# Kernel tuning notes

Measured on AMD Instinct MI355X. Metric: run time of the kernel, lower is better.

The kernel has to match this reference:

```python
import jax, jax.numpy as jnp
import numpy as np

T, B, D, H = 512, 64, 1024, 8
DH = D // H
LN_EPS = 1e-5


def setup_inputs() -> dict:
    ks = jax.random.split(jax.random.key(0), 12)
    s = 1.0 / np.sqrt(D)
    return {
        "x_real": jax.random.normal(ks[0], (T, B, D), jnp.float32),
        "x_imag": jax.random.normal(ks[1], (T, B, D), jnp.float32),
        "value_state": jnp.zeros((B, H, DH), jnp.float32),
        "t": jnp.arange(T, dtype=jnp.int64) if jax.config.jax_enable_x64 else jnp.arange(T, dtype=jnp.int32),
        # ComplexLinear input_proj (bias=True): weight layout [out, in] like torch
        "Wr_in": jax.random.normal(ks[2], (D, D), jnp.float32) * s,
        "Wi_in": jax.random.normal(ks[3], (D, D), jnp.float32) * s,
        "br_in": jax.random.normal(ks[4], (D,), jnp.float32) * 0.01,
        "bi_in": jax.random.normal(ks[5], (D,), jnp.float32) * 0.01,
        # LayerNorm affine
        "ln_gamma": jnp.ones((D,), jnp.float32),
        "ln_beta": jnp.zeros((D,), jnp.float32),
        # QKV linear (bias=False), torch layout [3D, D]
        "W_qkv": jax.random.normal(ks[6], (3 * D, D), jnp.float32) * s,
        # per-head EMA gate logits: log(alpha/(1-alpha)) with alpha=0.9
        "log_alpha": jnp.full((H,), float(np.log(0.9 / 0.1)), jnp.float32),
        # ComplexLinear output_proj (bias=False)
        "Wr_out": jax.random.normal(ks[7], (D, D), jnp.float32) * s,
        "Wi_out": jax.random.normal(ks[8], (D, D), jnp.float32) * s,
    }


def reference(x_real, x_imag, value_state, t, Wr_in, Wi_in, br_in, bi_in,
              ln_gamma, ln_beta, W_qkv, log_alpha, Wr_out, Wi_out):
    scale = jnp.asarray(np.sqrt(DH), x_real.dtype)
    alpha = jax.nn.sigmoid(log_alpha)[None, :, None]  # [1,H,1]

    def step(state, xs):
        xr, xi = xs  # [B,D] each
        # ComplexLinear input projection
        pr = xr @ Wr_in.T - xi @ Wi_in.T + br_in
        pi = xr @ Wi_in.T + xi @ Wr_in.T + bi_in
        xc = pr + pi
        # LayerNorm over last dim
        mu = xc.mean(-1, keepdims=True)
        var = ((xc - mu) ** 2).mean(-1, keepdims=True)
        xc = (xc - mu) * jax.lax.rsqrt(var + LN_EPS) * ln_gamma + ln_beta
        # QKV
        qkv = (xc @ W_qkv.T).reshape(-1, 3, H, DH)
        q, k, v = qkv[:, 0], qkv[:, 1], qkv[:, 2]  # [B,H,DH]
        # per-head sigmoid-gated EMA state update
        new_state = alpha * v + (1.0 - alpha) * state
        gate = jax.nn.sigmoid(jnp.sum(q * k, axis=-1, keepdims=True) / scale)  # [B,H,1]
        retrieved = (gate * new_state).reshape(-1, D)
        # ComplexLinear output projection with zero imaginary input
        return new_state, (retrieved @ Wr_out.T, retrieved @ Wi_out.T)

    final_state, (out_real, out_imag) = jax.lax.scan(step, value_state, (x_real, x_imag))
    return out_real, out_imag, final_state
```

## Files before the change

kernel.cpp:

```cpp
#include <hip/hip_runtime.h>
#include <stdint.h>

#define T_DIM 512
#define B_DIM 64
#define D_DIM 1024
#define H_DIM 8
#define DH_DIM 128
#define MROWS (T_DIM * B_DIM)

typedef unsigned short u16;
typedef __attribute__((ext_vector_type(8))) __bf16 bf16x8;
typedef __attribute__((ext_vector_type(4))) float f32x4;
typedef __attribute__((ext_vector_type(16))) float f32x16;

__device__ __forceinline__ u16 f2bf(float f) {
  union { float f; uint32_t u; } v; v.f = f;
  uint32_t u = v.u;
  u += 0x7fffu + ((u >> 16) & 1u);
  return (u16)(u >> 16);
}
__device__ __forceinline__ float bf2f(u16 h) {
  union { uint32_t u; float f; } v; v.u = ((uint32_t)h) << 16;
  return v.f;
}

__device__ __forceinline__ void gload16(const void* g, void* l) {
  __builtin_amdgcn_global_load_lds(
      (const __attribute__((address_space(1))) uint32_t*)g,
      (__attribute__((address_space(3))) uint32_t*)l, 16, 0, 0);
}

#define SB()  __builtin_amdgcn_sched_barrier(0)
#define BAR() __builtin_amdgcn_s_barrier()
#define VM4() asm volatile("s_waitcnt vmcnt(4)" ::: "memory")


__global__ void cast_bf16_kernel(const float* __restrict__ in, u16* __restrict__ out, size_t n8) {
  size_t i = (size_t)blockIdx.x * blockDim.x + threadIdx.x;
  const size_t stride = (size_t)gridDim.x * blockDim.x;
  for (; i < n8; i += stride) {
    const float4 a = ((const float4*)in)[i * 2];
    const float4 b = ((const float4*)in)[i * 2 + 1];
    union { u16 h[8]; uint4 u; } o;
    o.h[0] = f2bf(a.x); o.h[1] = f2bf(a.y); o.h[2] = f2bf(a.z); o.h[3] = f2bf(a.w);
    o.h[4] = f2bf(b.x); o.h[5] = f2bf(b.y); o.h[6] = f2bf(b.z); o.h[7] = f2bf(b.w);
    ((uint4*)out)[i] = o.u;
  }
}

__global__ void prep_wc_kernel(const float* __restrict__ Wr, const float* __restrict__ Wi,
                               u16* __restrict__ Wc) {
  const int idx = blockIdx.x * 256 + threadIdx.x;
  const int n = idx >> 11;
  const int k = idx & 2047;
  const int kk = k & 1023;
  const float a = Wr[n * 1024 + kk], b = Wi[n * 1024 + kk];
  Wc[idx] = f2bf(k < 1024 ? a + b : a - b);
}

__global__ void prep_bc_kernel(const float* __restrict__ br, const float* __restrict__ bi,
                               float* __restrict__ bc) {
  const int i = blockIdx.x * 256 + threadIdx.x;
  if (i < D_DIM) bc[i] = br[i] + bi[i];
}


__device__ __forceinline__ void readF(bf16x8 (&d)[2][2], const u16* s, int rowoff, int la32, int puA) {
#pragma unroll
  for (int mf = 0; mf < 2; ++mf)
#pragma unroll
    for (int kk = 0; kk < 2; ++kk)
      d[mf][kk] = *(const bf16x8*)(s + (rowoff + mf * 32 + la32) * 32 + (puA ^ (kk << 4)));
}

__device__ __forceinline__ void mfma8(f32x16 (&acc)[4][2], const bf16x8 (&a)[2][2],
                                      const bf16x8 (&b)[2][2], int QM) {
#pragma unroll
  for (int kk = 0; kk < 2; ++kk)
#pragma unroll
    for (int mf = 0; mf < 2; ++mf)
#pragma unroll
      for (int nf = 0; nf < 2; ++nf)
        acc[QM * 2 + mf][nf] =
            __builtin_amdgcn_mfma_f32_32x32x16_bf16(a[mf][kk], b[nf][kk], acc[QM * 2 + mf][nf], 0, 0, 0);
}

template <int EPI>
__global__ __launch_bounds__(512, 2) void gemm256_kernel(
    const u16* __restrict__ A0, const u16* __restrict__ A1, int kSplit, int lda,
    const u16* __restrict__ Bw, int ldb,
    const float* __restrict__ bias,
    void* __restrict__ C0, void* __restrict__ C1, void* __restrict__ C2,
    int ldc, int K, int nColBlk)
{
  extern __shared__ u16 lds[];
  const int tid  = threadIdx.x;
  const int lane = tid & 63;
  const int w    = tid >> 6;
  const int wr   = w >> 2;
  const int wc   = w & 3;

  const int bid   = blockIdx.x;
  const int xcd   = bid & 7;
  const int local = bid >> 3;
  const int rowL  = local / nColBlk;
  const int colB  = local - rowL * nColBlk;
  const size_t rowBase = (size_t)(xcd * 16 + rowL) * 256;
  const size_t colBase = (size_t)colB * 256;

  f32x16 acc[4][2];
#pragma unroll
  for (int i = 0; i < 4; ++i)
#pragma unroll
    for (int j = 0; j < 2; ++j)
#pragma unroll
      for (int e = 0; e < 16; ++e) acc[i][j][e] = 0.f;

  const int NT = K >> 6;
  const int la32 = lane & 31;
  const int g2   = lane >> 5;
  const int f    = (la32 & 3) ^ ((la32 >> 2) & 3);
  const int puA  = ((g2 ^ f) << 3);

  auto stageA = [&](int buf, int ks, int t) {
    if (t >= NT) return;
    const int kb = t * 64;
    const u16* Ab; int kc;
    if (kb < kSplit) { Ab = A0; kc = kb; } else { Ab = A1; kc = kb - kSplit; }
    u16* dst = lds + buf * 32768 + ks * 8192;
#pragma unroll
    for (int i2 = 0; i2 < 2; ++i2) {
      const int l = i2 * 512 + tid, r = l >> 2, p = l & 3;
      const int lu = p ^ (r & 3) ^ ((r >> 2) & 3);
      gload16(Ab + (rowBase + r) * (size_t)lda + kc + ks * 32 + lu * 8, dst + l * 8);
    }
  };
  auto stageB = [&](int buf, int ks, int t) {
    if (t >= NT) return;
    const int kb = t * 64;
    u16* dst = lds + buf * 32768 + 16384 + ks * 8192;
#pragma unroll
    for (int i2 = 0; i2 < 2; ++i2) {
      const int l = i2 * 512 + tid, r = l >> 2, p = l & 3;
      const int lu = p ^ (r & 3) ^ ((r >> 2) & 3);
      gload16(Bw + (colBase + r) * (size_t)ldb + kb + ks * 32 + lu * 8, dst + l * 8);
    }
  };

  const u16* sA_b0k0 = lds;
  const u16* sA_b0k1 = lds + 8192;
  const u16* sB_b0k0 = lds + 16384;
  const u16* sB_b0k1 = lds + 16384 + 8192;
  const u16* sA_b1k0 = lds + 32768;
  const u16* sA_b1k1 = lds + 32768 + 8192;
  const u16* sB_b1k0 = lds + 32768 + 16384;
  const u16* sB_b1k1 = lds + 32768 + 16384 + 8192;
  const int rA0 = wr * 128;
  const int rA1 = wr * 128 + 64;
  const int rB  = wc * 64;

  stageA(0, 0, 0); stageB(0, 0, 0); stageA(0, 1, 0); stageB(0, 1, 0);
  stageA(1, 0, 1); stageB(1, 0, 1);
  VM4();
  SB(); BAR(); SB();

  bf16x8 a0[2][2], a1[2][2], bb[2][2];
  const int NIT = NT >> 1;
  for (int i = 0; i < NIT; ++i) {
    const int u = 2 * i, v = 2 * i + 1;
    readF(a0, sA_b0k0, rA0, la32, puA);
    readF(bb, sB_b0k0, rB,  la32, puA);
    readF(a1, sA_b0k0, rA1, la32, puA);
    stageA(1, 1, v);
    SB(); BAR(); SB();
    __builtin_amdgcn_s_setprio(1); mfma8(acc, a0, bb, 0); __builtin_amdgcn_s_setprio(0); SB();
    BAR(); SB();
    readF(a0, sA_b0k1, rA0, la32, puA);
    stageB(1, 1, v);
    SB(); BAR(); SB();
    __builtin_amdgcn_s_setprio(1); mfma8(acc, a1, bb, 1); __builtin_amdgcn_s_setprio(0); SB();
    BAR(); SB();
    readF(bb, sB_b0k1, rB,  la32, puA);
    readF(a1, sA_b0k1, rA1, la32, puA);
    stageA(0, 0, u + 2);
    SB(); BAR(); SB();
    __builtin_amdgcn_s_setprio(1); mfma8(acc, a0, bb, 0); __builtin_amdgcn_s_setprio(0); SB();
    BAR(); SB();
    stageB(0, 0, u + 2);
    SB(); BAR(); SB();
    __builtin_amdgcn_s_setprio(1); mfma8(acc, a1, bb, 1); __builtin_amdgcn_s_setprio(0); SB();
    VM4(); BAR(); SB();
    readF(a0, sA_b1k0, rA0, la32, puA);
    readF(bb, sB_b1k0, rB,  la32, puA);
    readF(a1, sA_b1k0, rA1, la32, puA);
    stageA(0, 1, u + 2);
    SB(); BAR(); SB();
    __builtin_amdgcn_s_setprio(1); mfma8(acc, a0, bb, 0); __builtin_amdgcn_s_setprio(0); SB();
    BAR(); SB();
    readF(a0, sA_b1k1, rA0, la32, puA);
    stageB(0, 1, u + 2);
    SB(); BAR(); SB();
    __builtin_amdgcn_s_setprio(1); mfma8(acc, a1, bb, 1); __builtin_amdgcn_s_setprio(0); SB();
    BAR(); SB();
    readF(bb, sB_b1k1, rB,  la32, puA);
    readF(a1, sA_b1k1, rA1, la32, puA);
    stageA(1, 0, v + 2);
    SB(); BAR(); SB();
    __builtin_amdgcn_s_setprio(1); mfma8(acc, a0, bb, 0); __builtin_amdgcn_s_setprio(0); SB();
    BAR(); SB();
    stageB(1, 0, v + 2);
    SB(); BAR(); SB();
    __builtin_amdgcn_s_setprio(1); mfma8(acc, a1, bb, 1); __builtin_amdgcn_s_setprio(0); SB();
    VM4(); BAR(); SB();
  }

  const int seg = (int)(colBase >> 10);
  const size_t colSeg = colBase & 1023;
  void* Cout;
  if (EPI == 3)      Cout = (seg == 0) ? C0 : (seg == 1) ? C1 : C2;
  else if (EPI == 2) Cout = (seg == 0) ? C0 : C1;
  else               Cout = C0;

#pragma unroll
  for (int mi = 0; mi < 4; ++mi)
#pragma unroll
    for (int ni = 0; ni < 2; ++ni) {
      const int cn = wc * 64 + ni * 32 + la32;
      const float badd = (EPI == 1) ? bias[colBase + cn] : 0.0f;
      const size_t col = colSeg + cn;
#pragma unroll
      for (int r = 0; r < 16; ++r) {
        const size_t row = rowBase + wr * 128 + mi * 32 + (r & 3) + 8 * (r >> 2) + 4 * g2;
        const float v = acc[mi][ni][r] + badd;
        if (EPI == 2) ((float*)Cout)[row * (size_t)ldc + col] = v;
        else          ((u16*)Cout)[row * (size_t)ldc + col] = f2bf(v);
      }
    }
}


__global__ __launch_bounds__(256) void ln_kernel(u16* __restrict__ xc,
    const float* __restrict__ gamma, const float* __restrict__ beta)
{
  const size_t row = blockIdx.x;
  u16* p = xc + row * D_DIM;
  const int tid = threadIdx.x;
  const int c = tid * 4;
  const uint2 raw = *(const uint2*)(p + c);
  const float v0 = bf2f((u16)(raw.x & 0xffff)), v1 = bf2f((u16)(raw.x >> 16));
  const float v2 = bf2f((u16)(raw.y & 0xffff)), v3 = bf2f((u16)(raw.y >> 16));
  float s = v0 + v1 + v2 + v3;
  float q = v0 * v0 + v1 * v1 + v2 * v2 + v3 * v3;
#pragma unroll
  for (int o = 32; o > 0; o >>= 1) { s += __shfl_xor(s, o); q += __shfl_xor(q, o); }
  __shared__ float red[8];
  if ((tid & 63) == 0) { red[(tid >> 6) * 2] = s; red[(tid >> 6) * 2 + 1] = q; }
  __syncthreads();
  s = red[0] + red[2] + red[4] + red[6];
  q = red[1] + red[3] + red[5] + red[7];
  const float mu = s * (1.0f / D_DIM);
  const float var = q * (1.0f / D_DIM) - mu * mu;
  const float rstd = 1.0f / sqrtf(var + 1e-5f);
  const float y0 = (v0 - mu) * rstd * gamma[c] + beta[c];
  const float y1 = (v1 - mu) * rstd * gamma[c + 1] + beta[c + 1];
  const float y2 = (v2 - mu) * rstd * gamma[c + 2] + beta[c + 2];
  const float y3 = (v3 - mu) * rstd * gamma[c + 3] + beta[c + 3];
  const uint32_t o0 = (uint32_t)f2bf(y0) | ((uint32_t)f2bf(y1) << 16);
  const uint32_t o1 = (uint32_t)f2bf(y2) | ((uint32_t)f2bf(y3) << 16);
  *(uint2*)(p + c) = make_uint2(o0, o1);
}


__global__ __launch_bounds__(256) void gate_kernel(
    const u16* __restrict__ Q, const u16* __restrict__ Kb, float* __restrict__ gate)
{
  const int gw = blockIdx.x * 4 + (threadIdx.x >> 6);
  const int lane = threadIdx.x & 63;
  const size_t row = (size_t)(gw >> 3);
  const int h = gw & 7;
  const size_t off = row * D_DIM + h * DH_DIM + lane * 2;
  const uint32_t qr = *(const uint32_t*)(Q + off);
  const uint32_t kr = *(const uint32_t*)(Kb + off);
  float d = bf2f((u16)(qr & 0xffff)) * bf2f((u16)(kr & 0xffff))
          + bf2f((u16)(qr >> 16))    * bf2f((u16)(kr >> 16));
#pragma unroll
  for (int o = 32; o > 0; o >>= 1) d += __shfl_xor(d, o);
  if (lane == 0) {
    const float x = d * 0.08838834764831845f;
    gate[gw] = 1.0f / (1.0f + expf(-x));
  }
}


__global__ __launch_bounds__(256) void scan_kernel(
    const u16* __restrict__ vb, const float* __restrict__ gate,
    const float* __restrict__ vstate, const float* __restrict__ log_alpha,
    u16* __restrict__ ret, float* __restrict__ fstate)
{
  const int gid = blockIdx.x * 256 + threadIdx.x;
  const int b = gid >> 10;
  const int c = gid & 1023;
  const int h = c >> 7;
  const float alpha = 1.0f / (1.0f + expf(-log_alpha[h]));
  const float oma = 1.0f - alpha;
  float state = vstate[gid];
  const u16* vp = vb + (size_t)b * D_DIM + c;
  u16* rp = ret + (size_t)b * D_DIM + c;
  const float* gp = gate + b * H_DIM + h;
#pragma unroll 4
  for (int t = 0; t < T_DIM; ++t) {
    const float v = bf2f(vp[(size_t)t * (B_DIM * D_DIM)]);
    const float g = gp[(size_t)t * (B_DIM * H_DIM)];
    state = alpha * v + oma * state;
    rp[(size_t)t * (B_DIM * D_DIM)] = f2bf(g * state);
  }
  fstate[gid] = state;
}


extern "C" void kernel_launch(void* const* d_in, const int* in_sizes, int n_in,
                              void* d_out, int out_size, void* d_ws, size_t ws_size,
                              hipStream_t stream) {
  const float* x_real      = (const float*)d_in[0];
  const float* x_imag      = (const float*)d_in[1];
  const float* value_state = (const float*)d_in[2];
  const float* Wr_in  = (const float*)d_in[4];
  const float* Wi_in  = (const float*)d_in[5];
  const float* br_in  = (const float*)d_in[6];
  const float* bi_in  = (const float*)d_in[7];
  const float* ln_g   = (const float*)d_in[8];
  const float* ln_b   = (const float*)d_in[9];
  const float* W_qkv  = (const float*)d_in[10];
  const float* log_alpha = (const float*)d_in[11];
  const float* Wr_out = (const float*)d_in[12];
  const float* Wi_out = (const float*)d_in[13];

  float* out_real = (float*)d_out;
  float* out_imag = out_real + (size_t)MROWS * D_DIM;
  float* fstate   = out_imag + (size_t)MROWS * D_DIM;

  u16* R0a = (u16*)d_out;
  u16* xc  = (u16*)((char*)d_out + (size_t)MROWS * D_DIM * 2);
  u16* Vb  = (u16*)out_imag;

  char* ws = (char*)d_ws;
  size_t off = 0;
  auto alloc = [&](size_t bytes) { void* p = ws + off; off += (bytes + 255) & ~(size_t)255; return p; };
  u16*   Wc    = (u16*)alloc((size_t)1024 * 2048 * 2);
  u16*   Wqkvb = (u16*)alloc((size_t)3072 * 1024 * 2);
  u16*   Wob   = (u16*)alloc((size_t)2048 * 1024 * 2);
  float* bc    = (float*)alloc((size_t)D_DIM * 4);
  u16*   R0b   = (u16*)alloc((size_t)MROWS * D_DIM * 2);
  float* gate  = (float*)alloc((size_t)MROWS * H_DIM * 4);

  const int LDSB = 131072;
  hipFuncSetAttribute((const void*)gemm256_kernel<1>, hipFuncAttributeMaxDynamicSharedMemorySize, LDSB);
  hipFuncSetAttribute((const void*)gemm256_kernel<2>, hipFuncAttributeMaxDynamicSharedMemorySize, LDSB);
  hipFuncSetAttribute((const void*)gemm256_kernel<3>, hipFuncAttributeMaxDynamicSharedMemorySize, LDSB);

  prep_wc_kernel<<<(1024 * 2048) / 256, 256, 0, stream>>>(Wr_in, Wi_in, Wc);
  prep_bc_kernel<<<4, 256, 0, stream>>>(br_in, bi_in, bc);
  cast_bf16_kernel<<<1536, 256, 0, stream>>>(W_qkv, Wqkvb, (size_t)3072 * 1024 / 8);
  cast_bf16_kernel<<<512, 256, 0, stream>>>(Wr_out, Wob, (size_t)1024 * 1024 / 8);
  cast_bf16_kernel<<<512, 256, 0, stream>>>(Wi_out, Wob + (size_t)1024 * 1024, (size_t)1024 * 1024 / 8);
  cast_bf16_kernel<<<4096, 256, 0, stream>>>(x_real, R0a, (size_t)MROWS * D_DIM / 8);
  cast_bf16_kernel<<<4096, 256, 0, stream>>>(x_imag, R0b, (size_t)MROWS * D_DIM / 8);

  gemm256_kernel<1><<<dim3(128 * 4), 512, LDSB, stream>>>(
      R0a, R0b, 1024, 1024, Wc, 2048, bc, xc, nullptr, nullptr, 1024, 2048, 4);
  ln_kernel<<<MROWS, 256, 0, stream>>>(xc, ln_g, ln_b);
  gemm256_kernel<3><<<dim3(128 * 12), 512, LDSB, stream>>>(
      xc, xc, 1024, 1024, Wqkvb, 1024, nullptr, R0a, R0b, Vb, 1024, 1024, 12);
  gate_kernel<<<(MROWS * H_DIM) / 4, 256, 0, stream>>>(R0a, R0b, gate);
  scan_kernel<<<(B_DIM * D_DIM) / 256, 256, 0, stream>>>(Vb, gate, value_state, log_alpha, R0b, fstate);
  gemm256_kernel<2><<<dim3(128 * 8), 512, LDSB, stream>>>(
      R0b, R0b, 1024, 1024, Wob, 1024, nullptr, out_real, out_imag, nullptr, 1024, 1024, 8);
}
```

Measured before the change: 753.3 us.

## Double-buffer B fragments and reschedule LDS reads in GEMM main loop

Splits the B-fragment register into even and odd copies so the next k-slice's B and A fragments can be read from LDS earlier, overlapping those reads with the preceding MFMA groups. Adds an earlier vmcnt(6) wait so the next buffer's data is guaranteed before it is read. Tail prefetches past the last tile now reload tile 0 instead of being skipped, which keeps the count of outstanding loads uniform for the fixed waitcnt values but adds redundant global traffic. The extra fragment registers raise VGPR pressure and could lower occupancy.

```diff
diff --git a/kernel.cpp b/kernel.cpp
--- a/kernel.cpp
+++ b/kernel.cpp
@@ -33,6 +33,9 @@
 #define SB()  __builtin_amdgcn_sched_barrier(0)
 #define BAR() __builtin_amdgcn_s_barrier()
 #define VM4() asm volatile("s_waitcnt vmcnt(4)" ::: "memory")
+#define VM6() asm volatile("s_waitcnt vmcnt(6)" ::: "memory")
+#define PRIO1() __builtin_amdgcn_s_setprio(1)
+#define PRIO0() __builtin_amdgcn_s_setprio(0)
 
 
 __global__ void cast_bf16_kernel(const float* __restrict__ in, u16* __restrict__ out, size_t n8) {
@@ -123,7 +126,7 @@
   const int puA  = ((g2 ^ f) << 3);
 
   auto stageA = [&](int buf, int ks, int t) {
-    if (t >= NT) return;
+    if (t >= NT) t = 0;
     const int kb = t * 64;
     const u16* Ab; int kc;
     if (kb < kSplit) { Ab = A0; kc = kb; } else { Ab = A1; kc = kb - kSplit; }
@@ -136,7 +139,7 @@
     }
   };
   auto stageB = [&](int buf, int ks, int t) {
-    if (t >= NT) return;
+    if (t >= NT) t = 0;
     const int kb = t * 64;
     u16* dst = lds + buf * 32768 + 16384 + ks * 8192;
 #pragma unroll
@@ -164,54 +167,57 @@
   VM4();
   SB(); BAR(); SB();
 
-  bf16x8 a0[2][2], a1[2][2], bb[2][2];
+  bf16x8 a0[2][2], a1[2][2], bbE[2][2], bbO[2][2];
   const int NIT = NT >> 1;
   for (int i = 0; i < NIT; ++i) {
     const int u = 2 * i, v = 2 * i + 1;
-    readF(a0, sA_b0k0, rA0, la32, puA);
-    readF(bb, sB_b0k0, rB,  la32, puA);
-    readF(a1, sA_b0k0, rA1, la32, puA);
+    readF(a0,  sA_b0k0, rA0, la32, puA);
+    readF(bbE, sB_b0k0, rB,  la32, puA);
+    readF(a1,  sA_b0k0, rA1, la32, puA);
     stageA(1, 1, v);
     SB(); BAR(); SB();
-    __builtin_amdgcn_s_setprio(1); mfma8(acc, a0, bb, 0); __builtin_amdgcn_s_setprio(0); SB();
-    BAR(); SB();
-    readF(a0, sA_b0k1, rA0, la32, puA);
+    PRIO1(); mfma8(acc, a0, bbE, 0); PRIO0(); SB();
+    BAR(); SB();
+    readF(a0,  sA_b0k1, rA0, la32, puA);
+    readF(bbO, sB_b0k1, rB,  la32, puA);
     stageB(1, 1, v);
     SB(); BAR(); SB();
-    __builtin_amdgcn_s_setprio(1); mfma8(acc, a1, bb, 1); __builtin_amdgcn_s_setprio(0); SB();
-    BAR(); SB();
-    readF(bb, sB_b0k1, rB,  la32, puA);
-    readF(a1, sA_b0k1, rA1, la32, puA);
+    PRIO1(); mfma8(acc, a1, bbE, 1); PRIO0(); SB();
+    BAR(); SB();
+    readF(a1,  sA_b0k1, rA1, la32, puA);
     stageA(0, 0, u + 2);
     SB(); BAR(); SB();
-    __builtin_amdgcn_s_setprio(1); mfma8(acc, a0, bb, 0); __builtin_amdgcn_s_setprio(0); SB();
-    BAR(); SB();
+    PRIO1(); mfma8(acc, a0, bbO, 0); PRIO0(); SB();
+    VM6();
+    BAR(); SB();
+    readF(a0,  sA_b1k0, rA0, la32, puA);
+    readF(bbE, sB_b1k0, rB,  la32, puA);
     stageB(0, 0, u + 2);
     SB(); BAR(); SB();
-    __builtin_amdgcn_s_setprio(1); mfma8(acc, a1, bb, 1); __builtin_amdgcn_s_setprio(0); SB();
-    VM4(); BAR(); SB();
-    readF(a0, sA_b1k0, rA0, la32, puA);
-    readF(bb, sB_b1k0, rB,  la32, puA);
-    readF(a1, sA_b1k0, rA1, la32, puA);
+    PRIO1(); mfma8(acc, a1, bbO, 1); PRIO0(); SB();
+    VM4();
+    BAR(); SB();
+    readF(a1,  sA_b1k0, rA1, la32, puA);
     stageA(0, 1, u + 2);
     SB(); BAR(); SB();
-    __builtin_amdgcn_s_setprio(1); mfma8(acc, a0, bb, 0); __builtin_amdgcn_s_setprio(0); SB();
-    BAR(); SB();
-    readF(a0, sA_b1k1, rA0, la32, puA);
+    PRIO1(); mfma8(acc, a0, bbE, 0); PRIO0(); SB();
+    BAR(); SB();
+    readF(a0,  sA_b1k1, rA0, la32, puA);
+    readF(bbO, sB_b1k1, rB,  la32, puA);
     stageB(0, 1, u + 2);
     SB(); BAR(); SB();
-    __builtin_amdgcn_s_setprio(1); mfma8(acc, a1, bb, 1); __builtin_amdgcn_s_setprio(0); SB();
-    BAR(); SB();
-    readF(bb, sB_b1k1, rB,  la32, puA);
-    readF(a1, sA_b1k1, rA1, la32, puA);
+    PRIO1(); mfma8(acc, a1, bbE, 1); PRIO0(); SB();
+    BAR(); SB();
+    readF(a1,  sA_b1k1, rA1, la32, puA);
     stageA(1, 0, v + 2);
     SB(); BAR(); SB();
-    __builtin_amdgcn_s_setprio(1); mfma8(acc, a0, bb, 0); __builtin_amdgcn_s_setprio(0); SB();
+    PRIO1(); mfma8(acc, a0, bbO, 0); PRIO0(); SB();
     BAR(); SB();
     stageB(1, 0, v + 2);
     SB(); BAR(); SB();
-    __builtin_amdgcn_s_setprio(1); mfma8(acc, a1, bb, 1); __builtin_amdgcn_s_setprio(0); SB();
-    VM4(); BAR(); SB();
+    PRIO1(); mfma8(acc, a1, bbO, 1); PRIO0(); SB();
+    VM4();
+    BAR(); SB();
   }
 
   const int seg = (int)(colBase >> 10);
```

Result: no change. 750.8 us (-0.3%).
